# Kernel optimization log

Hardware: AMD Instinct MI355X
Metric: run time of the kernel (lower is better)

Reference implementation:

```python
import jax, jax.numpy as jnp
import numpy as np

HIDDEN = 1152
PATCH = 16
POS_SIZE = 64
B = 16
NP_ = 4096
IN_DIM = 3 * PATCH * PATCH  # 768


def setup_inputs() -> dict:
    key = jax.random.key(0)
    k1, k2, k3, k4, k5 = jax.random.split(key, 5)
    pixel_values = jax.random.normal(k1, (B, NP_, IN_DIM), dtype=jnp.float32)
    pixel_position_ids = jax.random.randint(k2, (B, NP_, 2), 0, POS_SIZE, dtype=jnp.int64)
    padding_positions = jax.random.randint(k3, (B, NP_), 0, 2) > 0
    # learned params: nn.Linear(input_dim, hidden, bias=False) weight is [hidden, in_dim]
    W = jax.random.normal(k4, (HIDDEN, IN_DIM), dtype=jnp.float32) / np.sqrt(IN_DIM)
    table = jax.random.normal(k5, (2, POS_SIZE, HIDDEN), dtype=jnp.float32)
    return {
        "pixel_values": pixel_values,
        "pixel_position_ids": pixel_position_ids,
        "padding_positions": padding_positions,
        "W": W,
        "table": table,
    }


def reference(pixel_values, pixel_position_ids, padding_positions, W, table):
    # input_proj: [B, N, in_dim] @ W.T -> [B, N, hidden]
    hidden_states = jnp.einsum("bnd,hd->bnh", pixel_values, W)
    # one_hot + matmul + sum over axis-of-2 is exactly a gather of the x-row
    # from table[0] plus the y-row from table[1]
    pos = jnp.clip(pixel_position_ids, 0, None)  # [B, N, 2]
    pe = table[0][pos[..., 0]] + table[1][pos[..., 1]]  # [B, N, hidden]
    pe = jnp.where(padding_positions[..., None], jnp.zeros_like(pe), pe)
    return hidden_states + pe
```

## Files before the change

kernel.cpp:

```cpp
#include <hip/hip_runtime.h>

#define HIDDEN 1152
#define IN_DIM 768
#define POS_SIZE 64
#define M_TOTAL (16 * 4096)

#define BM 64
#define NPASS 9
#define NSTAGE 12
#define TOTSTAGE (NPASS * NSTAGE)

typedef _Float16 f16x8 __attribute__((ext_vector_type(8)));
typedef float f32x4 __attribute__((ext_vector_type(4)));
typedef float f32x8v __attribute__((ext_vector_type(8)));

typedef __attribute__((address_space(1))) const void global_cv;
typedef __attribute__((address_space(3))) void lds_v;

__device__ __forceinline__ void async16(const void* g, void* l) {
    __builtin_amdgcn_global_load_lds((global_cv*)g, (lds_v*)l, 16, 0, 0);
}

__global__ __launch_bounds__(256) void pack_w(const float* __restrict__ W,
                                              _Float16* __restrict__ Wp) {
    unsigned tid = blockIdx.x * 256 + threadIdx.x;
    unsigned n = tid / 96u;
    unsigned kc = tid - n * 96u;
    f32x8v x = *(const f32x8v*)(W + (size_t)n * IN_DIM + kc * 8u);
    f16x8 h = __builtin_convertvector(x, f16x8);
    unsigned c = (n >> 4) * 1536u + kc * 16u + (n & 15u);
    ((f16x8*)Wp)[c] = h;
}

__device__ __forceinline__ void stageB(const f16x8* wp, _Float16* dstBuf,
                                       int t, int g) {
    int p = g / NSTAGE;
    int s = g - p * NSTAGE;
#pragma unroll
    for (int i = 0; i < 2; i++) {
        int c = t + i * 512;
        int kk = c >> 9;
        int n16l = (c >> 6) & 7;
        int lc = c & 63;
        size_t srcIdx = (size_t)(p * 8 + n16l) * 1536 + (size_t)(2 * s + kk) * 64 + lc;
        async16(wp + srcIdx, dstBuf + (size_t)c * 8);
    }
}

__global__ __launch_bounds__(512, 2) void gemm_pe(
    const float* __restrict__ A,
    const _Float16* __restrict__ Wp,
    const int* __restrict__ pos,
    const int* __restrict__ pad,
    const float* __restrict__ table,
    float* __restrict__ out) {
    __shared__ __align__(16) _Float16 sA[6144 * 8];
    __shared__ __align__(16) _Float16 sB[3][8192];

    const int m0 = blockIdx.x * BM;
    const int t = threadIdx.x;
    const int lane = t & 63;
    const int w = t >> 6;
    const int quad = lane >> 4;
    const int l15 = lane & 15;
    const int mw = w >> 2;
    const int nw = w & 3;

    const f16x8* wp = (const f16x8*)Wp;

    stageB(wp, sB[0], t, 0);
    stageB(wp, sB[1], t, 1);

    int pxv[8], pyv[8], pdv[8];
#pragma unroll
    for (int mi = 0; mi < 2; mi++)
#pragma unroll
        for (int r = 0; r < 4; r++) {
            const int gm = m0 + mw * 32 + mi * 16 + quad * 4 + r;
            int px = pos[gm * 2];
            int py = pos[gm * 2 + 1];
            pxv[mi * 4 + r] = px < 0 ? 0 : px;
            pyv[mi * 4 + r] = py < 0 ? 0 : py;
            pdv[mi * 4 + r] = pad[gm];
        }

    {
        const float* gA = A + (size_t)m0 * IN_DIM;
#pragma unroll 4
        for (int i = 0; i < 12; i++) {
            int c = t + i * 512;
            int row = c / 96;
            int kc = c - row * 96;
            f32x8v x = *(const f32x8v*)(gA + (size_t)row * IN_DIM + kc * 8);
            f16x8 h = __builtin_convertvector(x, f16x8);
            int chunk = kc * 64 + (row ^ ((kc & 7) << 1));
            *(f16x8*)&sA[(size_t)chunk * 8] = h;
        }
    }
    __syncthreads();

    const int arow_base = mw * 32 + l15;

    for (int pass = 0; pass < NPASS; pass++) {
        f32x4 acc[2][2];
#pragma unroll
        for (int mi = 0; mi < 2; mi++)
#pragma unroll
            for (int ni = 0; ni < 2; ni++) acc[mi][ni] = (f32x4)0.f;

        for (int s = 0; s < NSTAGE; s++) {
            const int g = pass * NSTAGE + s;
            if (g < TOTSTAGE - 2) {
                const int g2 = g + 2;
                stageB(wp, sB[g2 - (g2 / 3) * 3], t, g2);
                asm volatile("s_waitcnt vmcnt(4)" ::: "memory");
            } else if (g == TOTSTAGE - 2) {
                asm volatile("s_waitcnt vmcnt(2)" ::: "memory");
            } else {
                asm volatile("s_waitcnt vmcnt(0)" ::: "memory");
            }
            asm volatile("s_barrier" ::: "memory");

            const _Float16* bbuf = sB[g - (g / 3) * 3];
            f16x8 af[2][2], bf[2][2];
#pragma unroll
            for (int mi = 0; mi < 2; mi++)
#pragma unroll
                for (int kk = 0; kk < 2; kk++) {
                    const int kc = (2 * s + kk) * 4 + quad;
                    const int row = (arow_base + mi * 16) ^ ((kc & 7) << 1);
                    af[mi][kk] = *(const f16x8*)&sA[(size_t)(kc * 64 + row) * 8];
                }
#pragma unroll
            for (int ni = 0; ni < 2; ni++)
#pragma unroll
                for (int kk = 0; kk < 2; kk++)
                    bf[ni][kk] = *(const f16x8*)&bbuf[(size_t)((kk * 8 + nw * 2 + ni) * 64 +
                                                               lane) * 8];

            __builtin_amdgcn_s_setprio(1);
#pragma unroll
            for (int kk = 0; kk < 2; kk++)
#pragma unroll
                for (int mi = 0; mi < 2; mi++)
#pragma unroll
                    for (int ni = 0; ni < 2; ni++)
                        acc[mi][ni] = __builtin_amdgcn_mfma_f32_16x16x32_f16(
                            af[mi][kk], bf[ni][kk], acc[mi][ni], 0, 0, 0);
            __builtin_amdgcn_s_setprio(0);
            asm volatile("s_barrier" ::: "memory");
        }

        const int gn0 = pass * 128 + nw * 32;
#pragma unroll
        for (int mi = 0; mi < 2; mi++) {
#pragma unroll
            for (int r = 0; r < 4; r++) {
                const int gm = m0 + mw * 32 + mi * 16 + quad * 4 + r;
                const int idx = mi * 4 + r;
                const float* rx = table + (size_t)pxv[idx] * HIDDEN;
                const float* ry = table + (size_t)(POS_SIZE + pyv[idx]) * HIDDEN;
                float* orow = out + (size_t)gm * HIDDEN;
                const int isPad = pdv[idx];
#pragma unroll
                for (int ni = 0; ni < 2; ni++) {
                    const int gn = gn0 + ni * 16 + l15;
                    float pe = isPad ? 0.f : (rx[gn] + ry[gn]);
                    orow[gn] = acc[mi][ni][r] + pe;
                }
            }
        }
    }
}

__global__ __launch_bounds__(256) void fallback_naive(const float* __restrict__ A,
                                                      const float* __restrict__ W,
                                                      const int* __restrict__ pos,
                                                      const int* __restrict__ pad,
                                                      const float* __restrict__ table,
                                                      float* __restrict__ out) {
    long idx = (long)blockIdx.x * 256 + threadIdx.x;
    const long total = (long)M_TOTAL * HIDDEN;
    if (idx >= total) return;
    int m = (int)(idx / HIDDEN);
    int n = (int)(idx - (long)m * HIDDEN);
    const float* a = A + (size_t)m * IN_DIM;
    const float* wv = W + (size_t)n * IN_DIM;
    float s = 0.f;
    for (int k = 0; k < IN_DIM; k++) s += a[k] * wv[k];
    int px = pos[m * 2]; if (px < 0) px = 0;
    int py = pos[m * 2 + 1]; if (py < 0) py = 0;
    float pe = pad[m] ? 0.f : (table[(size_t)px * HIDDEN + n] +
                               table[(size_t)(POS_SIZE + py) * HIDDEN + n]);
    out[idx] = s + pe;
}

extern "C" void kernel_launch(void* const* d_in, const int* in_sizes, int n_in,
                              void* d_out, int out_size, void* d_ws, size_t ws_size,
                              hipStream_t stream) {
    const float* pixel = (const float*)d_in[0];
    const int* pos = (const int*)d_in[1];
    const int* pad = (const int*)d_in[2];
    const float* W = (const float*)d_in[3];
    const float* table = (const float*)d_in[4];
    float* out = (float*)d_out;

    const size_t nW = (size_t)HIDDEN * IN_DIM;
    if (ws_size >= nW * sizeof(_Float16)) {
        _Float16* Wp = (_Float16*)d_ws;
        pack_w<<<432, 256, 0, stream>>>(W, Wp);
        gemm_pe<<<M_TOTAL / BM, 512, 0, stream>>>(pixel, Wp, pos, pad, table, out);
    } else {
        long total = (long)M_TOTAL * HIDDEN;
        fallback_naive<<<(int)((total + 255) / 256), 256, 0, stream>>>(pixel, W, pos, pad,
                                                                       table, out);
    }
}
```

Measured before the change: 616.4 us.

## Give each wave a private B slice to drop block-wide barriers in GEMM loop

Each of the eight waves now owns a 16-column slice of every 128-column pass and loads its own W tile into a private triple-buffered LDS region. Because no wave reads another wave's B data, both per-stage s_barriers are removed and each wave relies only on its own vmcnt waits. Each wave now covers all 64 rows, so it issues twice as many A-fragment LDS reads per MFMA as before and keeps 4 accumulators. The position metadata is packed into one int per row to save registers.

```diff
diff --git a/kernel.cpp b/kernel.cpp
--- a/kernel.cpp
+++ b/kernel.cpp
@@ -32,21 +32,6 @@
     ((f16x8*)Wp)[c] = h;
 }
 
-__device__ __forceinline__ void stageB(const f16x8* wp, _Float16* dstBuf,
-                                       int t, int g) {
-    int p = g / NSTAGE;
-    int s = g - p * NSTAGE;
-#pragma unroll
-    for (int i = 0; i < 2; i++) {
-        int c = t + i * 512;
-        int kk = c >> 9;
-        int n16l = (c >> 6) & 7;
-        int lc = c & 63;
-        size_t srcIdx = (size_t)(p * 8 + n16l) * 1536 + (size_t)(2 * s + kk) * 64 + lc;
-        async16(wp + srcIdx, dstBuf + (size_t)c * 8);
-    }
-}
-
 __global__ __launch_bounds__(512, 2) void gemm_pe(
     const float* __restrict__ A,
     const _Float16* __restrict__ Wp,
@@ -55,7 +40,7 @@
     const float* __restrict__ table,
     float* __restrict__ out) {
     __shared__ __align__(16) _Float16 sA[6144 * 8];
-    __shared__ __align__(16) _Float16 sB[3][8192];
+    __shared__ __align__(16) _Float16 sB[8 * 3 * 1024];
 
     const int m0 = blockIdx.x * BM;
     const int t = threadIdx.x;
@@ -63,25 +48,28 @@
     const int w = t >> 6;
     const int quad = lane >> 4;
     const int l15 = lane & 15;
-    const int mw = w >> 2;
-    const int nw = w & 3;
 
     const f16x8* wp = (const f16x8*)Wp;
+    _Float16* myB = &sB[w * 3072];
 
-    stageB(wp, sB[0], t, 0);
-    stageB(wp, sB[1], t, 1);
+#pragma unroll
+    for (int g = 0; g < 2; ++g)
+#pragma unroll
+        for (int kk = 0; kk < 2; ++kk)
+            async16(wp + (size_t)(w * 1536 + (2 * g + kk) * 64 + lane),
+                    myB + (g * 1024 + kk * 512));
 
-    int pxv[8], pyv[8], pdv[8];
+    int meta[16];
 #pragma unroll
-    for (int mi = 0; mi < 2; mi++)
+    for (int mi = 0; mi < 4; mi++)
 #pragma unroll
         for (int r = 0; r < 4; r++) {
-            const int gm = m0 + mw * 32 + mi * 16 + quad * 4 + r;
+            const int gm = m0 + mi * 16 + quad * 4 + r;
             int px = pos[gm * 2];
             int py = pos[gm * 2 + 1];
-            pxv[mi * 4 + r] = px < 0 ? 0 : px;
-            pyv[mi * 4 + r] = py < 0 ? 0 : py;
-            pdv[mi * 4 + r] = pad[gm];
+            px = px < 0 ? 0 : px;
+            py = py < 0 ? 0 : py;
+            meta[mi * 4 + r] = px | (py << 8) | ((pad[gm] ? 1 : 0) << 16);
         }
 
     {
@@ -99,77 +87,70 @@
     }
     __syncthreads();
 
-    const int arow_base = mw * 32 + l15;
-
     for (int pass = 0; pass < NPASS; pass++) {
-        f32x4 acc[2][2];
+        f32x4 acc[4];
 #pragma unroll
-        for (int mi = 0; mi < 2; mi++)
-#pragma unroll
-            for (int ni = 0; ni < 2; ni++) acc[mi][ni] = (f32x4)0.f;
+        for (int mi = 0; mi < 4; mi++) acc[mi] = (f32x4)0.f;
 
         for (int s = 0; s < NSTAGE; s++) {
             const int g = pass * NSTAGE + s;
             if (g < TOTSTAGE - 2) {
                 const int g2 = g + 2;
-                stageB(wp, sB[g2 - (g2 / 3) * 3], t, g2);
+                const int p2 = g2 / NSTAGE;
+                const int s2 = g2 - p2 * NSTAGE;
+                const int slot2 = g2 - (g2 / 3) * 3;
+#pragma unroll
+                for (int kk = 0; kk < 2; ++kk)
+                    async16(wp + (size_t)(p2 * 12288 + w * 1536 + (2 * s2 + kk) * 64 + lane),
+                            myB + (slot2 * 1024 + kk * 512));
                 asm volatile("s_waitcnt vmcnt(4)" ::: "memory");
             } else if (g == TOTSTAGE - 2) {
                 asm volatile("s_waitcnt vmcnt(2)" ::: "memory");
             } else {
                 asm volatile("s_waitcnt vmcnt(0)" ::: "memory");
             }
-            asm volatile("s_barrier" ::: "memory");
 
-            const _Float16* bbuf = sB[g - (g / 3) * 3];
-            f16x8 af[2][2], bf[2][2];
+            const int slot = g - (g / 3) * 3;
+            f16x8 bf[2];
 #pragma unroll
-            for (int mi = 0; mi < 2; mi++)
+            for (int kk = 0; kk < 2; ++kk)
+                bf[kk] = *(const f16x8*)&myB[slot * 1024 + kk * 512 + lane * 8];
+
+            f16x8 af[4][2];
+#pragma unroll
+            for (int mi = 0; mi < 4; mi++)
 #pragma unroll
                 for (int kk = 0; kk < 2; kk++) {
                     const int kc = (2 * s + kk) * 4 + quad;
-                    const int row = (arow_base + mi * 16) ^ ((kc & 7) << 1);
+                    const int row = (l15 + mi * 16) ^ ((kc & 7) << 1);
                     af[mi][kk] = *(const f16x8*)&sA[(size_t)(kc * 64 + row) * 8];
                 }
-#pragma unroll
-            for (int ni = 0; ni < 2; ni++)
-#pragma unroll
-                for (int kk = 0; kk < 2; kk++)
-                    bf[ni][kk] = *(const f16x8*)&bbuf[(size_t)((kk * 8 + nw * 2 + ni) * 64 +
-                                                               lane) * 8];
 
             __builtin_amdgcn_s_setprio(1);
 #pragma unroll
             for (int kk = 0; kk < 2; kk++)
 #pragma unroll
-                for (int mi = 0; mi < 2; mi++)
-#pragma unroll
-                    for (int ni = 0; ni < 2; ni++)
-                        acc[mi][ni] = __builtin_amdgcn_mfma_f32_16x16x32_f16(
-                            af[mi][kk], bf[ni][kk], acc[mi][ni], 0, 0, 0);
+                for (int mi = 0; mi < 4; mi++)
+                    acc[mi] = __builtin_amdgcn_mfma_f32_16x16x32_f16(af[mi][kk], bf[kk],
+                                                                     acc[mi], 0, 0, 0);
             __builtin_amdgcn_s_setprio(0);
-            asm volatile("s_barrier" ::: "memory");
         }
 
-        const int gn0 = pass * 128 + nw * 32;
+        const int gn = pass * 128 + w * 16 + l15;
 #pragma unroll
-        for (int mi = 0; mi < 2; mi++) {
+        for (int mi = 0; mi < 4; mi++)
 #pragma unroll
             for (int r = 0; r < 4; r++) {
-                const int gm = m0 + mw * 32 + mi * 16 + quad * 4 + r;
-                const int idx = mi * 4 + r;
-                const float* rx = table + (size_t)pxv[idx] * HIDDEN;
-                const float* ry = table + (size_t)(POS_SIZE + pyv[idx]) * HIDDEN;
-                float* orow = out + (size_t)gm * HIDDEN;
-                const int isPad = pdv[idx];
-#pragma unroll
-                for (int ni = 0; ni < 2; ni++) {
-                    const int gn = gn0 + ni * 16 + l15;
-                    float pe = isPad ? 0.f : (rx[gn] + ry[gn]);
-                    orow[gn] = acc[mi][ni][r] + pe;
-                }
+                const int gm = m0 + mi * 16 + quad * 4 + r;
+                const int mv = meta[mi * 4 + r];
+                const int px = mv & 255;
+                const int py = (mv >> 8) & 255;
+                const int isPad = mv >> 16;
+                float pe = isPad ? 0.f
+                                 : (table[(size_t)px * HIDDEN + gn] +
+                                    table[(size_t)(POS_SIZE + py) * HIDDEN + gn]);
+                out[(size_t)gm * HIDDEN + gn] = acc[mi][r] + pe;
             }
-        }
     }
 }
 
```

Result: faster. 597.6 us (-3.1%).
